# Kernel tuning notes

Measured on AMD Instinct MI355X. Metric: run time of the kernel, lower is better.

Reference implementation:

```python
import jax, jax.numpy as jnp
import numpy as np

B, S, D = 4, 4096, 1024


def setup_inputs() -> dict:
    key = jax.random.key(0)
    ks = jax.random.split(key, 4)
    scale = 1.0 / np.sqrt(D)
    x = jax.random.normal(ks[0], (B, S, D), dtype=jnp.float32)
    Wg = jax.random.normal(ks[1], (D, D), dtype=jnp.float32) * scale
    Wv = jax.random.normal(ks[2], (D, D), dtype=jnp.float32) * scale
    Wd = jax.random.normal(ks[3], (D, D), dtype=jnp.float32) * scale
    bg = jnp.zeros((D,), dtype=jnp.float32)
    bv = jnp.zeros((D,), dtype=jnp.float32)
    bd = jnp.ones((D,), dtype=jnp.float32)  # decay_bias_init = 1.0
    return {"x": x, "Wg": Wg, "bg": bg, "Wv": Wv, "bv": bv, "Wd": Wd, "bd": bd}


def _scan_causal(x_scan, a):
    # h_t = a_t * h_{t-1} + x_t, scanned over time; x_scan, a: [B,S,D]
    def step(h, inp):
        a_t, x_t = inp
        h = a_t * h + x_t
        return h, h

    h0 = jnp.zeros(x_scan.shape[::2], dtype=x_scan.dtype)  # [B,D]
    xs = (jnp.swapaxes(a, 0, 1), jnp.swapaxes(x_scan, 0, 1))  # [S,B,D]
    _, out = jax.lax.scan(step, h0, xs)
    return jnp.swapaxes(out, 0, 1)  # back to [B,S,D]


def reference(x, Wg, bg, Wv, bv, Wd, bd):
    # nn.Linear: y = x @ W.T + b
    g = jnp.einsum('bsd,ed->bse', x, Wg) + bg
    v = jnp.einsum('bsd,ed->bse', x, Wv) + bv
    d = jnp.einsum('bsd,ed->bse', x, Wd) + bd
    x_scan = jax.nn.sigmoid(g) * jnp.tanh(v)
    a = 0.001 + 0.998 * jax.nn.sigmoid(d)
    return _scan_causal(x_scan, a)
```

## Files before the change

kernel.cpp:

```cpp
#include <hip/hip_runtime.h>
#include <cstddef>
#include <cstdint>


typedef _Float16 f16;
typedef f16 f16x8 __attribute__((ext_vector_type(8)));
typedef float f32x4 __attribute__((ext_vector_type(4)));

#define S_LEN 4096
#define D_DIM 1024
#define B_DIM 4
#define M_TOT (B_DIM * S_LEN)
#define N_TOT (3 * D_DIM)
#define K_TOT D_DIM

#define CLEN 16
#define CPB (S_LEN / CLEN)
#define NCHUNK (B_DIM * CPB)

__device__ __forceinline__ void cvt8(const float* s, f16* d) {
  f32x4 a = *(const f32x4*)s;
  f32x4 b = *(const f32x4*)(s + 4);
  f16x8 o;
  o[0] = (f16)a[0]; o[1] = (f16)a[1]; o[2] = (f16)a[2]; o[3] = (f16)a[3];
  o[4] = (f16)b[0]; o[5] = (f16)b[1]; o[6] = (f16)b[2]; o[7] = (f16)b[3];
  *(f16x8*)d = o;
}

__global__ void cvt_all_kernel(const float* __restrict__ x, const float* __restrict__ w0,
                               const float* __restrict__ w1, const float* __restrict__ w2,
                               f16* __restrict__ Ah, f16* __restrict__ Bh) {
  int i = (blockIdx.x * 256 + threadIdx.x) * 8;
  if (i < M_TOT * K_TOT) {
    cvt8(x + i, Ah + i);
  } else {
    int w = i - M_TOT * K_TOT;
    int row = w >> 10;
    int col = w & 1023;
    int srow = row / 3;
    int mat = row - srow * 3;
    const float* s = (mat == 0) ? w0 : (mat == 1) ? w1 : w2;
    cvt8(s + srow * 1024 + col, Bh + w);
  }
}

#define BM 128
#define BN 96
#define BK 32
#define RAWP 100
#define XSP 32

__device__ __forceinline__ void gl_lds16(const void* g, void* l) {
  __builtin_amdgcn_global_load_lds((const __attribute__((address_space(1))) void*)g,
                                   (__attribute__((address_space(3))) void*)l, 16, 0, 0);
}

__device__ __forceinline__ void act(float g, float v, float d, f16& xh, f16& ah) {
  float sg = 1.f / (1.f + __expf(-g));
  float tv = 1.f - 2.f / (__expf(2.f * v) + 1.f);
  float sd = 1.f / (1.f + __expf(-d));
  xh = (f16)(sg * tv);
  ah = (f16)(0.001f + 0.998f * sd);
}

__global__ __launch_bounds__(256) void gemm_fused_kernel(
    const f16* __restrict__ A, const f16* __restrict__ Bt,
    const float* __restrict__ bg, const float* __restrict__ bv,
    const float* __restrict__ bd,
    f16* __restrict__ xsA, f16* __restrict__ aA,
    float* __restrict__ P, float* __restrict__ H) {
  __shared__ __attribute__((aligned(16))) f16 smem[20992];
  f16* As = smem;
  f16* Bs = smem + 4096;
  const int tid = threadIdx.x;
  const int lane = tid & 63;
  const int wave = tid >> 6;
  const int m0 = blockIdx.y * BM;
  const int bn0 = blockIdx.x * BN;

  const int srow = tid >> 2;
  const int scol = (tid & 3) * 8;
  const f16* aG0 = A + (size_t)(m0 + srow) * K_TOT + scol;
  const f16* aG1 = A + (size_t)(m0 + srow + 64) * K_TOT + scol;
  const f16* bG0 = Bt + (size_t)(bn0 + srow) * K_TOT + scol;
  const f16* bG1 = Bt + (size_t)(bn0 + 64 + (tid >> 2)) * K_TOT + scol;
  f16* aL0 = As + tid * 8;
  f16* aL1 = As + 2048 + tid * 8;
  f16* bL0 = Bs + tid * 8;
  f16* bL1 = Bs + 2048 + tid * 8;

  const int wm = (wave >> 1) * 64;
  const int wn = (wave & 1) * 48;
  const int lm = lane & 15;
  const int kq = (lane >> 4) * 8;

  f32x4 acc[4][3] = {};

  for (int k0 = 0; k0 < K_TOT; k0 += BK) {
    gl_lds16(aG0 + k0, aL0);
    gl_lds16(aG1 + k0, aL1);
    gl_lds16(bG0 + k0, bL0);
    if (tid < 128) gl_lds16(bG1 + k0, bL1);
    __syncthreads();
    f16x8 af[4], bf[3];
#pragma unroll
    for (int i = 0; i < 4; ++i)
      af[i] = *(const f16x8*)&As[(wm + i * 16 + lm) * BK + kq];
#pragma unroll
    for (int j = 0; j < 3; ++j)
      bf[j] = *(const f16x8*)&Bs[(wn + j * 16 + lm) * BK + kq];
#pragma unroll
    for (int i = 0; i < 4; ++i)
#pragma unroll
      for (int j = 0; j < 3; ++j)
        acc[i][j] = __builtin_amdgcn_mfma_f32_16x16x32_f16(af[i], bf[j], acc[i][j], 0, 0, 0);
    __syncthreads();
  }

  f16* Raw = smem;
  const int r0 = wm + (lane >> 4) * 4;
  const int c0 = wn + (lane & 15);
#pragma unroll
  for (int i = 0; i < 4; ++i)
#pragma unroll
    for (int j = 0; j < 3; ++j)
#pragma unroll
      for (int r = 0; r < 4; ++r)
        Raw[(r0 + i * 16 + r) * RAWP + c0 + j * 16] = (f16)acc[i][j][r];
  __syncthreads();

  f16* xsL = smem + 12800;
  f16* aL = smem + 16896;
  {
    const int d = tid & 31;
    const int c = tid >> 5;
    const int gd = (blockIdx.x << 5) + d;
    const float Bg = bg[gd], Bv = bv[gd], Bd_ = bd[gd];
    float p = 1.f, h = 0.f;
#pragma unroll
    for (int i = 0; i < CLEN; ++i) {
      const int r = c * CLEN + i;
      const f16* t3 = &Raw[r * RAWP + 3 * d];
      f16 xh, ah;
      act((float)t3[0] + Bg, (float)t3[1] + Bv, (float)t3[2] + Bd_, xh, ah);
      xsL[r * XSP + d] = xh;
      aL[r * XSP + d] = ah;
      float xf = (float)xh, af_ = (float)ah;
      h = af_ * h + xf;
      p *= af_;
    }
    const int gs = (m0 >> 4) + c;
    P[(size_t)gs * D_DIM + gd] = p;
    H[(size_t)gs * D_DIM + gd] = h;
  }
  __syncthreads();

#pragma unroll
  for (int rr = 0; rr < 2; ++rr) {
    const int row = rr * 64 + (tid >> 2);
    const int col = (tid & 3) * 8;
    const size_t gi = (size_t)(m0 + row) * D_DIM + (blockIdx.x << 5) + col;
    *(f16x8*)(xsA + gi) = *(const f16x8*)&xsL[row * XSP + col];
    *(f16x8*)(aA + gi) = *(const f16x8*)&aL[row * XSP + col];
  }
}

__global__ void scan2_kernel(const float* __restrict__ P, const float* __restrict__ H,
                             float* __restrict__ carry) {
  const int idx = blockIdx.x * 256 + threadIdx.x;
  const int b = idx >> 10;
  const int d = idx & 1023;
  float h = 0.f;
  for (int c = 0; c < CPB; ++c) {
    int gs = b * CPB + c;
    carry[gs * D_DIM + d] = h;
    h = P[gs * D_DIM + d] * h + H[gs * D_DIM + d];
  }
}

__global__ void scan3_kernel(const f16* __restrict__ xsA, const f16* __restrict__ aA,
                             const float* __restrict__ carry, float* __restrict__ out) {
  const int u = blockIdx.x * 256 + threadIdx.x;
  const int cg = u & 127;
  const int b = (u >> 7) & 3;
  const int ck = u >> 9;
  const int ch = cg * 8;
  const int base = (b * CPB + ck) * D_DIM + ch;
  float h[8];
  *(f32x4*)h = *(const f32x4*)(carry + base);
  *(f32x4*)(h + 4) = *(const f32x4*)(carry + base + 4);
  const int t0 = ck * CLEN;
#pragma unroll 2
  for (int t = t0; t < t0 + CLEN; ++t) {
    const size_t m = (size_t)b * S_LEN + t;
    f16x8 xs8 = *(const f16x8*)(xsA + m * D_DIM + ch);
    f16x8 a8 = *(const f16x8*)(aA + m * D_DIM + ch);
#pragma unroll
    for (int j = 0; j < 8; ++j) h[j] = (float)a8[j] * h[j] + (float)xs8[j];
    float* op = out + m * D_DIM + ch;
    *(f32x4*)op = *(f32x4*)h;
    *(f32x4*)(op + 4) = *(f32x4*)(h + 4);
  }
}

extern "C" void kernel_launch(void* const* d_in, const int* in_sizes, int n_in,
                              void* d_out, int out_size, void* d_ws, size_t ws_size,
                              hipStream_t stream) {
  const float* x = (const float*)d_in[0];
  const float* Wg = (const float*)d_in[1];
  const float* bg = (const float*)d_in[2];
  const float* Wv = (const float*)d_in[3];
  const float* bv = (const float*)d_in[4];
  const float* Wd = (const float*)d_in[5];
  const float* bd = (const float*)d_in[6];
  float* out = (float*)d_out;

  char* ws = (char*)d_ws;
  f16* Ah = (f16*)(ws);
  f16* Bh = (f16*)(ws + 33554432);
  f16* xsA = (f16*)(ws + 39845888);
  f16* aA = (f16*)(ws + 73400320);
  float* P = (float*)(ws + 106954752);
  float* H = (float*)(ws + 111149056);
  float* carry = (float*)(ws + 115343360);

  cvt_all_kernel<<<9728, 256, 0, stream>>>(x, Wg, Wv, Wd, Ah, Bh);
  gemm_fused_kernel<<<dim3(N_TOT / BN, M_TOT / BM), 256, 0, stream>>>(
      Ah, Bh, bg, bv, bd, xsA, aA, P, H);
  scan2_kernel<<<16, 256, 0, stream>>>(P, H, carry);
  scan3_kernel<<<512, 256, 0, stream>>>(xsA, aA, carry, out);
}
```

Measured before the change: 332.7 us.

## Enlarge GEMM M tile with swizzled LDS and split chunk-carry scan into three levels

The GEMM block tile grows from 128 to 256 rows, each wave owns a 64x96 output slab, and the LDS K-offset is XOR-swizzled to cut bank conflicts. The fused epilogue now runs in two halves of 128 rows each. The serial carry scan, which used only 16 blocks over 256 chunks, becomes a segment reduce, a short serial scan over 16 segments, and a parallel expand, so far more threads work on it. In exchange there are more accumulator registers per thread, which may lower occupancy, and two extra kernel launches.

```diff
diff --git a/kernel.cpp b/kernel.cpp
--- a/kernel.cpp
+++ b/kernel.cpp
@@ -17,6 +17,9 @@
 #define CLEN 16
 #define CPB (S_LEN / CLEN)
 #define NCHUNK (B_DIM * CPB)
+
+#define SEG 16
+#define NSEG (CPB / SEG)
 
 __device__ __forceinline__ void cvt8(const float* s, f16* d) {
   f32x4 a = *(const f32x4*)s;
@@ -44,7 +47,7 @@
   }
 }
 
-#define BM 128
+#define BM 256
 #define BN 96
 #define BK 32
 #define RAWP 100
@@ -71,7 +74,7 @@
     float* __restrict__ P, float* __restrict__ H) {
   __shared__ __attribute__((aligned(16))) f16 smem[20992];
   f16* As = smem;
-  f16* Bs = smem + 4096;
+  f16* Bs = smem + 8192;
   const int tid = threadIdx.x;
   const int lane = tid & 63;
   const int wave = tid >> 6;
@@ -79,102 +82,143 @@
   const int bn0 = blockIdx.x * BN;
 
   const int srow = tid >> 2;
-  const int scol = (tid & 3) * 8;
-  const f16* aG0 = A + (size_t)(m0 + srow) * K_TOT + scol;
-  const f16* aG1 = A + (size_t)(m0 + srow + 64) * K_TOT + scol;
+  const int scol = (((tid & 3) ^ ((tid >> 3) & 3)) * 8);
+  const f16* aG = A + (size_t)(m0 + srow) * K_TOT + scol;
   const f16* bG0 = Bt + (size_t)(bn0 + srow) * K_TOT + scol;
-  const f16* bG1 = Bt + (size_t)(bn0 + 64 + (tid >> 2)) * K_TOT + scol;
-  f16* aL0 = As + tid * 8;
-  f16* aL1 = As + 2048 + tid * 8;
+  const f16* bG1 = Bt + (size_t)(bn0 + 64 + srow) * K_TOT + scol;
+  f16* aL = As + tid * 8;
   f16* bL0 = Bs + tid * 8;
   f16* bL1 = Bs + 2048 + tid * 8;
 
-  const int wm = (wave >> 1) * 64;
-  const int wn = (wave & 1) * 48;
+  const int wm = wave * 64;
   const int lm = lane & 15;
-  const int kq = (lane >> 4) * 8;
-
-  f32x4 acc[4][3] = {};
+  const int kswz = (((lane >> 4) ^ ((lm >> 1) & 3)) << 3);
+
+  f32x4 acc[4][6] = {};
 
   for (int k0 = 0; k0 < K_TOT; k0 += BK) {
-    gl_lds16(aG0 + k0, aL0);
-    gl_lds16(aG1 + k0, aL1);
+#pragma unroll
+    for (int r = 0; r < 4; ++r)
+      gl_lds16(aG + (size_t)r * 64 * K_TOT + k0, aL + r * 2048);
     gl_lds16(bG0 + k0, bL0);
     if (tid < 128) gl_lds16(bG1 + k0, bL1);
     __syncthreads();
-    f16x8 af[4], bf[3];
+    f16x8 af[4], bf[6];
 #pragma unroll
     for (int i = 0; i < 4; ++i)
-      af[i] = *(const f16x8*)&As[(wm + i * 16 + lm) * BK + kq];
-#pragma unroll
-    for (int j = 0; j < 3; ++j)
-      bf[j] = *(const f16x8*)&Bs[(wn + j * 16 + lm) * BK + kq];
+      af[i] = *(const f16x8*)&As[(wm + i * 16 + lm) * BK + kswz];
+#pragma unroll
+    for (int j = 0; j < 6; ++j)
+      bf[j] = *(const f16x8*)&Bs[(j * 16 + lm) * BK + kswz];
 #pragma unroll
     for (int i = 0; i < 4; ++i)
 #pragma unroll
-      for (int j = 0; j < 3; ++j)
+      for (int j = 0; j < 6; ++j)
         acc[i][j] = __builtin_amdgcn_mfma_f32_16x16x32_f16(af[i], bf[j], acc[i][j], 0, 0, 0);
     __syncthreads();
   }
 
   f16* Raw = smem;
-  const int r0 = wm + (lane >> 4) * 4;
-  const int c0 = wn + (lane & 15);
-#pragma unroll
-  for (int i = 0; i < 4; ++i)
-#pragma unroll
-    for (int j = 0; j < 3; ++j)
-#pragma unroll
-      for (int r = 0; r < 4; ++r)
-        Raw[(r0 + i * 16 + r) * RAWP + c0 + j * 16] = (f16)acc[i][j][r];
-  __syncthreads();
-
   f16* xsL = smem + 12800;
-  f16* aL = smem + 16896;
-  {
-    const int d = tid & 31;
-    const int c = tid >> 5;
-    const int gd = (blockIdx.x << 5) + d;
-    const float Bg = bg[gd], Bv = bv[gd], Bd_ = bd[gd];
-    float p = 1.f, h = 0.f;
-#pragma unroll
-    for (int i = 0; i < CLEN; ++i) {
-      const int r = c * CLEN + i;
-      const f16* t3 = &Raw[r * RAWP + 3 * d];
-      f16 xh, ah;
-      act((float)t3[0] + Bg, (float)t3[1] + Bv, (float)t3[2] + Bd_, xh, ah);
-      xsL[r * XSP + d] = xh;
-      aL[r * XSP + d] = ah;
-      float xf = (float)xh, af_ = (float)ah;
-      h = af_ * h + xf;
-      p *= af_;
+  f16* aLs = smem + 16896;
+  const int d = tid & 31;
+  const int cc = tid >> 5;
+  const int gd = (blockIdx.x << 5) + d;
+  const float Bg = bg[gd], Bv = bv[gd], Bd_ = bd[gd];
+
+#pragma unroll
+  for (int half = 0; half < 2; ++half) {
+    if ((wave >> 1) == half) {
+      const int r0 = (wave & 1) * 64 + ((lane >> 4) << 2);
+      const int c0 = lane & 15;
+#pragma unroll
+      for (int i = 0; i < 4; ++i)
+#pragma unroll
+        for (int j = 0; j < 6; ++j)
+#pragma unroll
+          for (int r = 0; r < 4; ++r)
+            Raw[(r0 + i * 16 + r) * RAWP + c0 + j * 16] = (f16)acc[i][j][r];
     }
-    const int gs = (m0 >> 4) + c;
-    P[(size_t)gs * D_DIM + gd] = p;
-    H[(size_t)gs * D_DIM + gd] = h;
-  }
-  __syncthreads();
-
-#pragma unroll
-  for (int rr = 0; rr < 2; ++rr) {
-    const int row = rr * 64 + (tid >> 2);
-    const int col = (tid & 3) * 8;
-    const size_t gi = (size_t)(m0 + row) * D_DIM + (blockIdx.x << 5) + col;
-    *(f16x8*)(xsA + gi) = *(const f16x8*)&xsL[row * XSP + col];
-    *(f16x8*)(aA + gi) = *(const f16x8*)&aL[row * XSP + col];
-  }
-}
-
-__global__ void scan2_kernel(const float* __restrict__ P, const float* __restrict__ H,
-                             float* __restrict__ carry) {
+    __syncthreads();
+
+    {
+      float p = 1.f, h = 0.f;
+#pragma unroll
+      for (int i = 0; i < CLEN; ++i) {
+        const int r = cc * CLEN + i;
+        const f16* t3 = &Raw[r * RAWP + 3 * d];
+        f16 xh, ah;
+        act((float)t3[0] + Bg, (float)t3[1] + Bv, (float)t3[2] + Bd_, xh, ah);
+        xsL[r * XSP + d] = xh;
+        aLs[r * XSP + d] = ah;
+        float xf = (float)xh, af_ = (float)ah;
+        h = af_ * h + xf;
+        p *= af_;
+      }
+      const int gs = (m0 >> 4) + half * 8 + cc;
+      P[(size_t)gs * D_DIM + gd] = p;
+      H[(size_t)gs * D_DIM + gd] = h;
+    }
+    __syncthreads();
+
+#pragma unroll
+    for (int rr = 0; rr < 2; ++rr) {
+      const int row = rr * 64 + (tid >> 2);
+      const int col = (tid & 3) * 8;
+      const size_t gi = (size_t)(m0 + half * 128 + row) * D_DIM + (blockIdx.x << 5) + col;
+      *(f16x8*)(xsA + gi) = *(const f16x8*)&xsL[row * XSP + col];
+      *(f16x8*)(aA + gi) = *(const f16x8*)&aLs[row * XSP + col];
+    }
+    __syncthreads();
+  }
+}
+
+__global__ void scan2a_kernel(const float* __restrict__ P, const float* __restrict__ H,
+                              float* __restrict__ SP, float* __restrict__ SH) {
+  const int u = blockIdx.x * 256 + threadIdx.x;
+  const int d = u & 1023;
+  const int s = (u >> 10) & (NSEG - 1);
+  const int b = u >> 14;
+  const int gs0 = b * CPB + s * SEG;
+  float p = 1.f, h = 0.f;
+#pragma unroll 4
+  for (int c = 0; c < SEG; ++c) {
+    const size_t off = (size_t)(gs0 + c) * D_DIM + d;
+    const float pp = P[off], hh = H[off];
+    h = pp * h + hh;
+    p *= pp;
+  }
+  const size_t so = (size_t)(b * NSEG + s) * D_DIM + d;
+  SP[so] = p;
+  SH[so] = h;
+}
+
+__global__ void scan2b_kernel(const float* __restrict__ SP, const float* __restrict__ SH,
+                              float* __restrict__ segC) {
   const int idx = blockIdx.x * 256 + threadIdx.x;
   const int b = idx >> 10;
   const int d = idx & 1023;
   float h = 0.f;
-  for (int c = 0; c < CPB; ++c) {
-    int gs = b * CPB + c;
-    carry[gs * D_DIM + d] = h;
-    h = P[gs * D_DIM + d] * h + H[gs * D_DIM + d];
+  for (int s = 0; s < NSEG; ++s) {
+    const size_t off = (size_t)(b * NSEG + s) * D_DIM + d;
+    segC[off] = h;
+    h = SP[off] * h + SH[off];
+  }
+}
+
+__global__ void scan2c_kernel(const float* __restrict__ P, const float* __restrict__ H,
+                              const float* __restrict__ segC, float* __restrict__ carry) {
+  const int u = blockIdx.x * 256 + threadIdx.x;
+  const int d = u & 1023;
+  const int s = (u >> 10) & (NSEG - 1);
+  const int b = u >> 14;
+  float h = segC[(size_t)(b * NSEG + s) * D_DIM + d];
+  const int gs0 = b * CPB + s * SEG;
+#pragma unroll 4
+  for (int c = 0; c < SEG; ++c) {
+    const size_t off = (size_t)(gs0 + c) * D_DIM + d;
+    carry[off] = h;
+    h = P[off] * h + H[off];
   }
 }
 
@@ -223,10 +267,15 @@
   float* P = (float*)(ws + 106954752);
   float* H = (float*)(ws + 111149056);
   float* carry = (float*)(ws + 115343360);
+  float* SP = (float*)(ws);
+  float* SH = (float*)(ws + 262144);
+  float* segC = (float*)(ws + 524288);
 
   cvt_all_kernel<<<9728, 256, 0, stream>>>(x, Wg, Wv, Wd, Ah, Bh);
   gemm_fused_kernel<<<dim3(N_TOT / BN, M_TOT / BM), 256, 0, stream>>>(
       Ah, Bh, bg, bv, bd, xsA, aA, P, H);
-  scan2_kernel<<<16, 256, 0, stream>>>(P, H, carry);
+  scan2a_kernel<<<256, 256, 0, stream>>>(P, H, SP, SH);
+  scan2b_kernel<<<16, 256, 0, stream>>>(SP, SH, segC);
+  scan2c_kernel<<<256, 256, 0, stream>>>(P, H, segC, carry);
   scan3_kernel<<<512, 256, 0, stream>>>(xsA, aA, carry, out);
 }
```

New measurement: 417.4 us. 1.25x slower.
